# Kernel tuning notes

Hardware: AMD Instinct MI355X
Metric: run time of the kernel (lower is better)

The kernel has to match this reference:

```python
import jax, jax.numpy as jnp
import numpy as np

N_TOK = 2048      # flattened batch*seq tokens
D_MODEL = 1024    # in_features
D_INT = 512       # d_intermediate
N_EXPERTS = 8     # n_routed_experts
TOP_K = 2         # n_activated_experts


def setup_inputs() -> dict:
    key = jax.random.key(0)
    k1, k2, k3, k4, k5 = jax.random.split(key, 5)
    x = jax.random.normal(k1, (N_TOK, D_MODEL), dtype=jnp.float32)
    indices = jax.random.randint(k2, (N_TOK, TOP_K), 0, N_EXPERTS, dtype=jnp.int32)
    # router combine weights (normalized over top-k like a softmax router)
    weights = jax.nn.softmax(jax.random.normal(k3, (N_TOK, TOP_K), dtype=jnp.float32), axis=-1)
    # tokens-per-expert counts, consistent with indices (as the router would supply)
    counts = jnp.bincount(indices.reshape(-1), length=N_EXPERTS).astype(jnp.int32)
    # expert weights: fc1 -> 2*d_int (gated MLP), fc2 -> d_model; kaiming-ish scale
    s1 = 1.0 / np.sqrt(D_MODEL)
    s2 = 1.0 / np.sqrt(D_INT)
    fc1_weight = jax.random.uniform(k4, (N_EXPERTS, 2 * D_INT, D_MODEL), jnp.float32, -s1, s1)
    fc2_weight = jax.random.uniform(k5, (N_EXPERTS, D_MODEL, D_INT), jnp.float32, -s2, s2)
    return {"x": x, "weights": weights, "indices": indices, "counts": counts,
            "fc1_weight": fc1_weight, "fc2_weight": fc2_weight}


def reference(x, weights, indices, counts, fc1_weight, fc2_weight):
    # Dense dispatch-free formulation: run every token through every expert's
    # gated MLP, then gather the per-slot expert output. Identical math to the
    # sort / grouped-GEMM / scatter path for the selected (token, expert) pairs.
    # h: (n_tok, n_experts, 2*d_int)
    h = jnp.einsum('td,egd->teg', x, fc1_weight)
    y, z = jnp.split(h, 2, axis=-1)
    a = y * jax.nn.silu(z)  # GatedMLP: y * activation(z)
    # expert outputs: (n_tok, n_experts, d_model)
    out = jnp.einsum('tei,edi->ted', a, fc2_weight)
    # gather the chosen expert output for each of the top-k slots: (n_tok, k, d_model)
    per_slot = jnp.take_along_axis(out, indices[:, :, None], axis=1)
    # combine: z = bmm(weights[:, None], x_by_expert).squeeze(1)
    return jnp.einsum('tk,tkd->td', weights, per_slot)
```

## Files before the change

### kernel.cpp

```cpp
#include <hip/hip_runtime.h>

typedef unsigned short u16;
typedef unsigned int u32;
using short8  = __attribute__((ext_vector_type(8))) short;
using floatx4 = __attribute__((ext_vector_type(4))) float;

#define N_TOK   2048
#define D_MODEL 1024
#define D_INT   512
#define NE      8
#define ROWS_PAD 5120

#define O_TOK    0
#define O_WROW   24576
#define O_XG     65536
#define O_ACT    10551296
#define O_FC1B   36765696
#define O_FC2B   53542912

static __device__ inline u16 f2bf(float f) {
    u32 u = __builtin_bit_cast(u32, f);
    u = (u + 0x7fffu + ((u >> 16) & 1u)) >> 16;
    return (u16)u;
}
static __device__ inline u32 pack2(float a, float b) {
    return (u32)f2bf(a) | ((u32)f2bf(b) << 16);
}
static __device__ inline void glds16(const u16* g, u16* l) {
    __builtin_amdgcn_global_load_lds(
        (const __attribute__((address_space(1))) void*)g,
        (__attribute__((address_space(3))) void*)l, 16, 0, 0);
}

__global__ __launch_bounds__(256) void prep_kernel(
    const float* __restrict__ x, const float* __restrict__ wts,
    const int* __restrict__ indices, const int* __restrict__ counts,
    const float* __restrict__ fc1, const float* __restrict__ fc2,
    u16* __restrict__ fc1b, u16* __restrict__ fc2b,
    u16* __restrict__ Xg, int* __restrict__ tok, float* __restrict__ wrow,
    float* __restrict__ out) {
    int b = blockIdx.x, tid = threadIdx.x;
    if (b < 6144) {
        size_t v = (size_t)b * 256 + tid;
        const float* src; u16* dst; size_t off;
        if (v < 1048576) { src = fc1; dst = fc1b; off = v * 8; }
        else             { src = fc2; dst = fc2b; off = (v - 1048576) * 8; }
        const floatx4* s4 = reinterpret_cast<const floatx4*>(src + off);
        floatx4 a = s4[0], bb = s4[1];
        uint4 o;
        o.x = pack2(a[0], a[1]); o.y = pack2(a[2], a[3]);
        o.z = pack2(bb[0], bb[1]); o.w = pack2(bb[2], bb[3]);
        *reinterpret_cast<uint4*>(dst + off) = o;
        return;
    }
    if (b < 8192) {
        int t = b - 6144;
        int off[NE];
        {
            int acc = 0;
            #pragma unroll
            for (int e = 0; e < NE; e++) { off[e] = acc; acc += ((counts[e] + 127) >> 7) << 7; }
        }
        int e0 = indices[2 * t], e1 = indices[2 * t + 1];
        __shared__ int s0, s1;
        if (tid == 0) { s0 = 0; s1 = 0; }
        __syncthreads();
        int c0 = 0, c1 = 0;
        const int4* ip = reinterpret_cast<const int4*>(indices);
        #pragma unroll
        for (int i = 0; i < 4; i++) {
            int4 vv = ip[tid * 4 + i];
            int q = tid * 16 + i * 4;
            c0 += (q + 0 < 2 * t && vv.x == e0) + (q + 1 < 2 * t && vv.y == e0)
                + (q + 2 < 2 * t && vv.z == e0) + (q + 3 < 2 * t && vv.w == e0);
            c1 += (q + 0 <= 2 * t && vv.x == e1) + (q + 1 <= 2 * t && vv.y == e1)
                + (q + 2 <= 2 * t && vv.z == e1) + (q + 3 <= 2 * t && vv.w == e1);
        }
        if (c0) atomicAdd(&s0, c0);
        if (c1) atomicAdd(&s1, c1);
        __syncthreads();
        int r0 = off[e0] + s0;
        int r1 = off[e1] + s1;
        if (tid == 0) {
            tok[r0] = t; tok[r1] = t;
            wrow[r0] = wts[2 * t]; wrow[r1] = wts[2 * t + 1];
        }
        const floatx4* src = reinterpret_cast<const floatx4*>(x + (size_t)t * D_MODEL);
        floatx4 a = src[tid];
        uint2 o;
        o.x = pack2(a[0], a[1]); o.y = pack2(a[2], a[3]);
        *reinterpret_cast<uint2*>(Xg + (size_t)r0 * D_MODEL + tid * 4) = o;
        *reinterpret_cast<uint2*>(Xg + (size_t)r1 * D_MODEL + tid * 4) = o;
        return;
    }
    {
        int z = b - 8192;
        floatx4* dst = reinterpret_cast<floatx4*>(out) + (size_t)z * 1024;
        #pragma unroll
        for (int i = 0; i < 4; i++) dst[i * 256 + tid] = (floatx4){0.f, 0.f, 0.f, 0.f};
        return;
    }
}

__global__ __launch_bounds__(256) void gemm1_kernel(
    const u16* __restrict__ Xg, const u16* __restrict__ fc1b,
    u16* __restrict__ Act, const int* __restrict__ counts) {
    __shared__ u16 As[4096];
    __shared__ u16 Bs[4096];
    int tid = threadIdx.x;
    int soff[NE + 1];
    {
        int acc = 0;
        #pragma unroll
        for (int e2 = 0; e2 < NE; e2++) { soff[e2] = acc; acc += ((counts[e2] + 127) >> 7) << 7; }
        soff[NE] = acc;
    }
    int row0 = blockIdx.y * 128;
    if (row0 >= soff[NE]) return;
    int e = 0;
    while (soff[e + 1] <= row0) e++;
    int bx = blockIdx.x;
    const u16* A  = Xg + (size_t)row0 * 1024;
    const u16* Be = fc1b + (size_t)e * 1024 * 1024;

    int lane = tid & 63, w = tid >> 6;
    int m0 = (w >> 1) * 64, n0 = (w & 1) * 32;
    int lr = lane & 15, kq = lane >> 4;
    int ka = ((kq ^ ((lr >> 1) & 3)) * 8);

    int v0 = tid, v1 = tid + 256;
    int r0s = v0 >> 2, kb0 = (v0 & 3) ^ ((r0s >> 1) & 3);
    int r1s = v1 >> 2, kb1 = (v1 & 3) ^ ((r1s >> 1) & 3);
    int brow0 = (r0s < 64) ? bx * 64 + r0s : 448 + bx * 64 + r0s;
    int brow1 = (r1s < 64) ? bx * 64 + r1s : 448 + bx * 64 + r1s;
    u16* lA0 = As + (w * 64) * 8;
    u16* lA1 = As + (w * 64 + 256) * 8;
    u16* lB0 = Bs + (w * 64) * 8;
    u16* lB1 = Bs + (w * 64 + 256) * 8;
    const u16* gA0 = A + (size_t)r0s * 1024 + kb0 * 8;
    const u16* gA1 = A + (size_t)r1s * 1024 + kb1 * 8;
    const u16* gB0 = Be + (size_t)brow0 * 1024 + kb0 * 8;
    const u16* gB1 = Be + (size_t)brow1 * 1024 + kb1 * 8;

    floatx4 acc[4][4];
    #pragma unroll
    for (int i = 0; i < 4; i++)
        #pragma unroll
        for (int j = 0; j < 4; j++) acc[i][j] = (floatx4){0.f, 0.f, 0.f, 0.f};

    for (int k0 = 0; k0 < 1024; k0 += 32) {
        glds16(gA0 + k0, lA0);
        glds16(gA1 + k0, lA1);
        glds16(gB0 + k0, lB0);
        glds16(gB1 + k0, lB1);
        __syncthreads();
        short8 af[4], bf[4];
        #pragma unroll
        for (int i = 0; i < 4; i++)
            af[i] = *reinterpret_cast<const short8*>(&As[(m0 + i * 16 + lr) * 32 + ka]);
        #pragma unroll
        for (int j = 0; j < 4; j++) {
            int nn = (j < 2) ? (n0 + j * 16) : (64 + n0 + (j - 2) * 16);
            bf[j] = *reinterpret_cast<const short8*>(&Bs[(nn + lr) * 32 + ka]);
        }
        #pragma unroll
        for (int i = 0; i < 4; i++)
            #pragma unroll
            for (int j = 0; j < 4; j++)
                acc[i][j] = __builtin_amdgcn_mfma_f32_16x16x32_bf16(af[i], bf[j], acc[i][j], 0, 0, 0);
        __syncthreads();
    }
    #pragma unroll
    for (int i = 0; i < 4; i++) {
        #pragma unroll
        for (int jy = 0; jy < 2; jy++) {
            floatx4 y = acc[i][jy], z = acc[i][jy + 2];
            #pragma unroll
            for (int r = 0; r < 4; r++) {
                float zz = z[r];
                float av = y[r] * (zz / (1.0f + __expf(-zz)));
                int m = m0 + i * 16 + kq * 4 + r;
                int g = bx * 64 + n0 + jy * 16 + lr;
                Act[(size_t)(row0 + m) * D_INT + g] = f2bf(av);
            }
        }
    }
}

__global__ __launch_bounds__(256) void gemm2_kernel(
    const u16* __restrict__ Act, const u16* __restrict__ fc2b,
    float* __restrict__ out, const int* __restrict__ counts,
    const int* __restrict__ tok, const float* __restrict__ wrow) {
    __shared__ u16 As[4096];
    __shared__ u16 Bs[4096];
    __shared__ int sTok[128];
    __shared__ float sW[128];
    int tid = threadIdx.x;
    int soff[NE + 1];
    int cnt[NE];
    {
        int acc = 0;
        #pragma unroll
        for (int e2 = 0; e2 < NE; e2++) {
            soff[e2] = acc; cnt[e2] = counts[e2];
            acc += ((cnt[e2] + 127) >> 7) << 7;
        }
        soff[NE] = acc;
    }
    int row0 = blockIdx.y * 128;
    if (row0 >= soff[NE]) return;
    int e = 0;
    while (soff[e + 1] <= row0) e++;
    int bx = blockIdx.x;
    const u16* A  = Act + (size_t)row0 * 512;
    const u16* Be = fc2b + (size_t)e * 1024 * 512;

    int lane = tid & 63, w = tid >> 6;
    int m0 = (w >> 1) * 64, n0 = (w & 1) * 64;
    int lr = lane & 15, kq = lane >> 4;
    int ka = ((kq ^ ((lr >> 1) & 3)) * 8);

    int v0 = tid, v1 = tid + 256;
    int r0s = v0 >> 2, kb0 = (v0 & 3) ^ ((r0s >> 1) & 3);
    int r1s = v1 >> 2, kb1 = (v1 & 3) ^ ((r1s >> 1) & 3);
    u16* lA0 = As + (w * 64) * 8;
    u16* lA1 = As + (w * 64 + 256) * 8;
    u16* lB0 = Bs + (w * 64) * 8;
    u16* lB1 = Bs + (w * 64 + 256) * 8;
    const u16* gA0 = A + (size_t)r0s * 512 + kb0 * 8;
    const u16* gA1 = A + (size_t)r1s * 512 + kb1 * 8;
    const u16* gB0 = Be + (size_t)(bx * 128 + r0s) * 512 + kb0 * 8;
    const u16* gB1 = Be + (size_t)(bx * 128 + r1s) * 512 + kb1 * 8;

    floatx4 acc[4][4];
    #pragma unroll
    for (int i = 0; i < 4; i++)
        #pragma unroll
        for (int j = 0; j < 4; j++) acc[i][j] = (floatx4){0.f, 0.f, 0.f, 0.f};

    for (int k0 = 0; k0 < 512; k0 += 32) {
        glds16(gA0 + k0, lA0);
        glds16(gA1 + k0, lA1);
        glds16(gB0 + k0, lB0);
        glds16(gB1 + k0, lB1);
        __syncthreads();
        short8 af[4], bf[4];
        #pragma unroll
        for (int i = 0; i < 4; i++)
            af[i] = *reinterpret_cast<const short8*>(&As[(m0 + i * 16 + lr) * 32 + ka]);
        #pragma unroll
        for (int j = 0; j < 4; j++)
            bf[j] = *reinterpret_cast<const short8*>(&Bs[(n0 + j * 16 + lr) * 32 + ka]);
        #pragma unroll
        for (int i = 0; i < 4; i++)
            #pragma unroll
            for (int j = 0; j < 4; j++)
                acc[i][j] = __builtin_amdgcn_mfma_f32_16x16x32_bf16(af[i], bf[j], acc[i][j], 0, 0, 0);
        __syncthreads();
    }
    if (tid < 128) {
        int g = row0 + tid;
        bool val = (g - soff[e]) < cnt[e];
        sTok[tid] = val ? tok[g] : -1;
        sW[tid]   = val ? wrow[g] : 0.f;
    }
    __syncthreads();
    #pragma unroll
    for (int i = 0; i < 4; i++)
        #pragma unroll
        for (int r = 0; r < 4; r++) {
            int m = m0 + i * 16 + kq * 4 + r;
            int t = sTok[m];
            if (t >= 0) {
                float wgt = sW[m];
                float* dst = out + (size_t)t * D_MODEL + bx * 128;
                #pragma unroll
                for (int j = 0; j < 4; j++)
                    atomicAdd(dst + n0 + j * 16 + lr, wgt * acc[i][j][r]);
            }
        }
}

extern "C" void kernel_launch(void* const* d_in, const int* in_sizes, int n_in,
                              void* d_out, int out_size, void* d_ws, size_t ws_size,
                              hipStream_t stream) {
    const float* x       = (const float*)d_in[0];
    const float* wts     = (const float*)d_in[1];
    const int*   indices = (const int*)d_in[2];
    const int*   counts  = (const int*)d_in[3];
    const float* fc1     = (const float*)d_in[4];
    const float* fc2     = (const float*)d_in[5];
    float* out = (float*)d_out;
    char* ws = (char*)d_ws;

    int*   tok  = (int*)(ws + O_TOK);
    float* wrow = (float*)(ws + O_WROW);
    u16*   Xg   = (u16*)(ws + O_XG);
    u16*   Act  = (u16*)(ws + O_ACT);
    u16*   fc1b = (u16*)(ws + O_FC1B);
    u16*   fc2b = (u16*)(ws + O_FC2B);

    prep_kernel<<<8704, 256, 0, stream>>>(x, wts, indices, counts, fc1, fc2,
                                          fc1b, fc2b, Xg, tok, wrow, out);
    gemm1_kernel<<<dim3(8, 40), 256, 0, stream>>>(Xg, fc1b, Act, counts);
    gemm2_kernel<<<dim3(8, 40), 256, 0, stream>>>(Act, fc2b, out, counts, tok, wrow);
}
```

Baseline: 159.1 us.

## Shrink expert row tiles to 64 and deepen K tile to 64 in both GEMMs

Expert row padding drops from 128 to 64 rows, so less padded work is done and there are more row blocks (72 instead of 40) to fill the GPU. Each K step now loads a 64-wide slice with a new XOR swizzle over 8 chunks, which halves the number of barrier iterations. The per-wave tiles are smaller, so each loaded B tile is reused across fewer rows and B traffic per output rises.

```diff
diff --git a/kernel.cpp b/kernel.cpp
--- a/kernel.cpp
+++ b/kernel.cpp
@@ -9,7 +9,6 @@
 #define D_MODEL 1024
 #define D_INT   512
 #define NE      8
-#define ROWS_PAD 5120
 
 #define O_TOK    0
 #define O_WROW   24576
@@ -59,7 +58,7 @@
         {
             int acc = 0;
             #pragma unroll
-            for (int e = 0; e < NE; e++) { off[e] = acc; acc += ((counts[e] + 127) >> 7) << 7; }
+            for (int e = 0; e < NE; e++) { off[e] = acc; acc += ((counts[e] + 63) >> 6) << 6; }
         }
         int e0 = indices[2 * t], e1 = indices[2 * t + 1];
         __shared__ int s0, s1;
@@ -105,17 +104,17 @@
 __global__ __launch_bounds__(256) void gemm1_kernel(
     const u16* __restrict__ Xg, const u16* __restrict__ fc1b,
     u16* __restrict__ Act, const int* __restrict__ counts) {
-    __shared__ u16 As[4096];
-    __shared__ u16 Bs[4096];
+    __shared__ u16 As[64 * 64];
+    __shared__ u16 Bs[128 * 64];
     int tid = threadIdx.x;
     int soff[NE + 1];
     {
         int acc = 0;
         #pragma unroll
-        for (int e2 = 0; e2 < NE; e2++) { soff[e2] = acc; acc += ((counts[e2] + 127) >> 7) << 7; }
+        for (int e2 = 0; e2 < NE; e2++) { soff[e2] = acc; acc += ((counts[e2] + 63) >> 6) << 6; }
         soff[NE] = acc;
     }
-    int row0 = blockIdx.y * 128;
+    int row0 = blockIdx.y * 64;
     if (row0 >= soff[NE]) return;
     int e = 0;
     while (soff[e + 1] <= row0) e++;
@@ -124,90 +123,96 @@
     const u16* Be = fc1b + (size_t)e * 1024 * 1024;
 
     int lane = tid & 63, w = tid >> 6;
-    int m0 = (w >> 1) * 64, n0 = (w & 1) * 32;
+    int m0 = (w >> 1) * 32, n0 = (w & 1) * 32;
     int lr = lane & 15, kq = lane >> 4;
-    int ka = ((kq ^ ((lr >> 1) & 3)) * 8);
-
-    int v0 = tid, v1 = tid + 256;
-    int r0s = v0 >> 2, kb0 = (v0 & 3) ^ ((r0s >> 1) & 3);
-    int r1s = v1 >> 2, kb1 = (v1 & 3) ^ ((r1s >> 1) & 3);
-    int brow0 = (r0s < 64) ? bx * 64 + r0s : 448 + bx * 64 + r0s;
-    int brow1 = (r1s < 64) ? bx * 64 + r1s : 448 + bx * 64 + r1s;
-    u16* lA0 = As + (w * 64) * 8;
-    u16* lA1 = As + (w * 64 + 256) * 8;
-    u16* lB0 = Bs + (w * 64) * 8;
-    u16* lB1 = Bs + (w * 64 + 256) * 8;
-    const u16* gA0 = A + (size_t)r0s * 1024 + kb0 * 8;
-    const u16* gA1 = A + (size_t)r1s * 1024 + kb1 * 8;
-    const u16* gB0 = Be + (size_t)brow0 * 1024 + kb0 * 8;
-    const u16* gB1 = Be + (size_t)brow1 * 1024 + kb1 * 8;
-
-    floatx4 acc[4][4];
-    #pragma unroll
-    for (int i = 0; i < 4; i++)
-        #pragma unroll
-        for (int j = 0; j < 4; j++) acc[i][j] = (floatx4){0.f, 0.f, 0.f, 0.f};
-
-    for (int k0 = 0; k0 < 1024; k0 += 32) {
-        glds16(gA0 + k0, lA0);
-        glds16(gA1 + k0, lA1);
-        glds16(gB0 + k0, lB0);
-        glds16(gB1 + k0, lB1);
-        __syncthreads();
-        short8 af[4], bf[4];
-        #pragma unroll
-        for (int i = 0; i < 4; i++)
-            af[i] = *reinterpret_cast<const short8*>(&As[(m0 + i * 16 + lr) * 32 + ka]);
-        #pragma unroll
-        for (int j = 0; j < 4; j++) {
-            int nn = (j < 2) ? (n0 + j * 16) : (64 + n0 + (j - 2) * 16);
-            bf[j] = *reinterpret_cast<const short8*>(&Bs[(nn + lr) * 32 + ka]);
-        }
-        #pragma unroll
-        for (int i = 0; i < 4; i++)
-            #pragma unroll
-            for (int j = 0; j < 4; j++)
-                acc[i][j] = __builtin_amdgcn_mfma_f32_16x16x32_bf16(af[i], bf[j], acc[i][j], 0, 0, 0);
-        __syncthreads();
-    }
-    #pragma unroll
-    for (int i = 0; i < 4; i++) {
-        #pragma unroll
-        for (int jy = 0; jy < 2; jy++) {
-            floatx4 y = acc[i][jy], z = acc[i][jy + 2];
+
+    const u16* gA[2]; u16* lA[2];
+    #pragma unroll
+    for (int j = 0; j < 2; j++) {
+        int v = tid + j * 256;
+        int r = v >> 3, kb = (v & 7) ^ (r & 7);
+        gA[j] = A + (size_t)r * 1024 + kb * 8;
+        lA[j] = As + (w * 64 + j * 256) * 8;
+    }
+    const u16* gB[4]; u16* lB[4];
+    #pragma unroll
+    for (int j = 0; j < 4; j++) {
+        int v = tid + j * 256;
+        int r = v >> 3, kb = (v & 7) ^ (r & 7);
+        int grow = (r < 64) ? (bx * 64 + r) : (448 + bx * 64 + r);
+        gB[j] = Be + (size_t)grow * 1024 + kb * 8;
+        lB[j] = Bs + (w * 64 + j * 256) * 8;
+    }
+
+    floatx4 aY[2][2], aZ[2][2];
+    #pragma unroll
+    for (int i = 0; i < 2; i++)
+        #pragma unroll
+        for (int j = 0; j < 2; j++) {
+            aY[i][j] = (floatx4){0.f, 0.f, 0.f, 0.f};
+            aZ[i][j] = (floatx4){0.f, 0.f, 0.f, 0.f};
+        }
+
+    for (int k0 = 0; k0 < 1024; k0 += 64) {
+        glds16(gA[0] + k0, lA[0]); glds16(gA[1] + k0, lA[1]);
+        glds16(gB[0] + k0, lB[0]); glds16(gB[1] + k0, lB[1]);
+        glds16(gB[2] + k0, lB[2]); glds16(gB[3] + k0, lB[3]);
+        __syncthreads();
+        #pragma unroll
+        for (int ks = 0; ks < 2; ks++) {
+            int sw = ((ks * 4 + kq) ^ (lr & 7)) * 8;
+            short8 af[2], by[2], bz[2];
+            #pragma unroll
+            for (int i = 0; i < 2; i++)
+                af[i] = *reinterpret_cast<const short8*>(&As[(m0 + i * 16 + lr) * 64 + sw]);
+            #pragma unroll
+            for (int j = 0; j < 2; j++) {
+                by[j] = *reinterpret_cast<const short8*>(&Bs[(n0 + j * 16 + lr) * 64 + sw]);
+                bz[j] = *reinterpret_cast<const short8*>(&Bs[(64 + n0 + j * 16 + lr) * 64 + sw]);
+            }
+            #pragma unroll
+            for (int i = 0; i < 2; i++)
+                #pragma unroll
+                for (int j = 0; j < 2; j++) {
+                    aY[i][j] = __builtin_amdgcn_mfma_f32_16x16x32_bf16(af[i], by[j], aY[i][j], 0, 0, 0);
+                    aZ[i][j] = __builtin_amdgcn_mfma_f32_16x16x32_bf16(af[i], bz[j], aZ[i][j], 0, 0, 0);
+                }
+        }
+        __syncthreads();
+    }
+    #pragma unroll
+    for (int i = 0; i < 2; i++)
+        #pragma unroll
+        for (int j = 0; j < 2; j++) {
+            floatx4 y = aY[i][j], z = aZ[i][j];
             #pragma unroll
             for (int r = 0; r < 4; r++) {
                 float zz = z[r];
                 float av = y[r] * (zz / (1.0f + __expf(-zz)));
                 int m = m0 + i * 16 + kq * 4 + r;
-                int g = bx * 64 + n0 + jy * 16 + lr;
+                int g = bx * 64 + n0 + j * 16 + lr;
                 Act[(size_t)(row0 + m) * D_INT + g] = f2bf(av);
             }
         }
-    }
 }
 
 __global__ __launch_bounds__(256) void gemm2_kernel(
     const u16* __restrict__ Act, const u16* __restrict__ fc2b,
     float* __restrict__ out, const int* __restrict__ counts,
     const int* __restrict__ tok, const float* __restrict__ wrow) {
-    __shared__ u16 As[4096];
-    __shared__ u16 Bs[4096];
-    __shared__ int sTok[128];
-    __shared__ float sW[128];
+    __shared__ u16 As[64 * 64];
+    __shared__ u16 Bs[128 * 64];
+    __shared__ int sTok[64];
+    __shared__ float sW[64];
     int tid = threadIdx.x;
     int soff[NE + 1];
-    int cnt[NE];
     {
         int acc = 0;
         #pragma unroll
-        for (int e2 = 0; e2 < NE; e2++) {
-            soff[e2] = acc; cnt[e2] = counts[e2];
-            acc += ((cnt[e2] + 127) >> 7) << 7;
-        }
+        for (int e2 = 0; e2 < NE; e2++) { soff[e2] = acc; acc += ((counts[e2] + 63) >> 6) << 6; }
         soff[NE] = acc;
     }
-    int row0 = blockIdx.y * 128;
+    int row0 = blockIdx.y * 64;
     if (row0 >= soff[NE]) return;
     int e = 0;
     while (soff[e + 1] <= row0) e++;
@@ -216,57 +221,64 @@
     const u16* Be = fc2b + (size_t)e * 1024 * 512;
 
     int lane = tid & 63, w = tid >> 6;
-    int m0 = (w >> 1) * 64, n0 = (w & 1) * 64;
+    int m0 = (w >> 1) * 32, n0 = (w & 1) * 64;
     int lr = lane & 15, kq = lane >> 4;
-    int ka = ((kq ^ ((lr >> 1) & 3)) * 8);
-
-    int v0 = tid, v1 = tid + 256;
-    int r0s = v0 >> 2, kb0 = (v0 & 3) ^ ((r0s >> 1) & 3);
-    int r1s = v1 >> 2, kb1 = (v1 & 3) ^ ((r1s >> 1) & 3);
-    u16* lA0 = As + (w * 64) * 8;
-    u16* lA1 = As + (w * 64 + 256) * 8;
-    u16* lB0 = Bs + (w * 64) * 8;
-    u16* lB1 = Bs + (w * 64 + 256) * 8;
-    const u16* gA0 = A + (size_t)r0s * 512 + kb0 * 8;
-    const u16* gA1 = A + (size_t)r1s * 512 + kb1 * 8;
-    const u16* gB0 = Be + (size_t)(bx * 128 + r0s) * 512 + kb0 * 8;
-    const u16* gB1 = Be + (size_t)(bx * 128 + r1s) * 512 + kb1 * 8;
-
-    floatx4 acc[4][4];
-    #pragma unroll
-    for (int i = 0; i < 4; i++)
+
+    const u16* gA[2]; u16* lA[2];
+    #pragma unroll
+    for (int j = 0; j < 2; j++) {
+        int v = tid + j * 256;
+        int r = v >> 3, kb = (v & 7) ^ (r & 7);
+        gA[j] = A + (size_t)r * 512 + kb * 8;
+        lA[j] = As + (w * 64 + j * 256) * 8;
+    }
+    const u16* gB[4]; u16* lB[4];
+    #pragma unroll
+    for (int j = 0; j < 4; j++) {
+        int v = tid + j * 256;
+        int r = v >> 3, kb = (v & 7) ^ (r & 7);
+        gB[j] = Be + (size_t)(bx * 128 + r) * 512 + kb * 8;
+        lB[j] = Bs + (w * 64 + j * 256) * 8;
+    }
+
+    floatx4 acc[2][4];
+    #pragma unroll
+    for (int i = 0; i < 2; i++)
         #pragma unroll
         for (int j = 0; j < 4; j++) acc[i][j] = (floatx4){0.f, 0.f, 0.f, 0.f};
 
-    for (int k0 = 0; k0 < 512; k0 += 32) {
-        glds16(gA0 + k0, lA0);
-        glds16(gA1 + k0, lA1);
-        glds16(gB0 + k0, lB0);
-        glds16(gB1 + k0, lB1);
-        __syncthreads();
-        short8 af[4], bf[4];
-        #pragma unroll
-        for (int i = 0; i < 4; i++)
-            af[i] = *reinterpret_cast<const short8*>(&As[(m0 + i * 16 + lr) * 32 + ka]);
-        #pragma unroll
-        for (int j = 0; j < 4; j++)
-            bf[j] = *reinterpret_cast<const short8*>(&Bs[(n0 + j * 16 + lr) * 32 + ka]);
-        #pragma unroll
-        for (int i = 0; i < 4; i++)
+    for (int k0 = 0; k0 < 512; k0 += 64) {
+        glds16(gA[0] + k0, lA[0]); glds16(gA[1] + k0, lA[1]);
+        glds16(gB[0] + k0, lB[0]); glds16(gB[1] + k0, lB[1]);
+        glds16(gB[2] + k0, lB[2]); glds16(gB[3] + k0, lB[3]);
+        __syncthreads();
+        #pragma unroll
+        for (int ks = 0; ks < 2; ks++) {
+            int sw = ((ks * 4 + kq) ^ (lr & 7)) * 8;
+            short8 af[2], bf[4];
+            #pragma unroll
+            for (int i = 0; i < 2; i++)
+                af[i] = *reinterpret_cast<const short8*>(&As[(m0 + i * 16 + lr) * 64 + sw]);
             #pragma unroll
             for (int j = 0; j < 4; j++)
-                acc[i][j] = __builtin_amdgcn_mfma_f32_16x16x32_bf16(af[i], bf[j], acc[i][j], 0, 0, 0);
-        __syncthreads();
-    }
-    if (tid < 128) {
+                bf[j] = *reinterpret_cast<const short8*>(&Bs[(n0 + j * 16 + lr) * 64 + sw]);
+            #pragma unroll
+            for (int i = 0; i < 2; i++)
+                #pragma unroll
+                for (int j = 0; j < 4; j++)
+                    acc[i][j] = __builtin_amdgcn_mfma_f32_16x16x32_bf16(af[i], bf[j], acc[i][j], 0, 0, 0);
+        }
+        __syncthreads();
+    }
+    if (tid < 64) {
         int g = row0 + tid;
-        bool val = (g - soff[e]) < cnt[e];
+        bool val = (g - soff[e]) < counts[e];
         sTok[tid] = val ? tok[g] : -1;
         sW[tid]   = val ? wrow[g] : 0.f;
     }
     __syncthreads();
     #pragma unroll
-    for (int i = 0; i < 4; i++)
+    for (int i = 0; i < 2; i++)
         #pragma unroll
         for (int r = 0; r < 4; r++) {
             int m = m0 + i * 16 + kq * 4 + r;
@@ -302,6 +314,6 @@
 
     prep_kernel<<<8704, 256, 0, stream>>>(x, wts, indices, counts, fc1, fc2,
                                           fc1b, fc2b, Xg, tok, wrow, out);
-    gemm1_kernel<<<dim3(8, 40), 256, 0, stream>>>(Xg, fc1b, Act, counts);
-    gemm2_kernel<<<dim3(8, 40), 256, 0, stream>>>(Act, fc2b, out, counts, tok, wrow);
-}
+    gemm1_kernel<<<dim3(8, 72), 256, 0, stream>>>(Xg, fc1b, Act, counts);
+    gemm2_kernel<<<dim3(8, 72), 256, 0, stream>>>(Act, fc2b, out, counts, tok, wrow);
+}
```

New measurement: 151.6 us. 4.7% less time.
